# Optimization experiments

Hardware: AMD Instinct MI355X
Metric: run time of the kernel (lower is better)

Reference implementation:

```python
import jax, jax.numpy as jnp
import numpy as np


def setup_inputs() -> dict:
    key = jax.random.key(0)
    kq, kk, kv = jax.random.split(key, 3)
    B, L, H, E = 2, 2048, 16, 64
    queries = jax.random.normal(kq, (B, L, H, E), dtype=jnp.float32)
    keys = jax.random.normal(kk, (B, L, H, E), dtype=jnp.float32)
    values = jax.random.normal(kv, (B, L, H, E), dtype=jnp.float32)
    return {"queries": queries, "keys": keys, "values": values}


def reference(queries, keys, values):
    # queries: [B, L, H, E], keys: [B, S, H, E], values: [B, S, H, D]
    B, L, H, E = queries.shape
    S = keys.shape[1]
    scale = 1.0 / jnp.sqrt(jnp.asarray(E, dtype=queries.dtype))
    # scores: [B, H, L, S]
    scores = jnp.einsum('blhe,bshe->bhls', queries, keys)
    # TriangularCausalMask: mask out strictly-upper-triangular (future) positions
    causal = jnp.triu(jnp.ones((L, S), dtype=bool), k=1)
    neg_inf = jnp.asarray(-jnp.inf, dtype=scores.dtype)
    scores = jnp.where(causal[None, None, :, :], neg_inf, scores)
    A = jax.nn.softmax(scale * scores, axis=-1)  # dropout p=0.0 (eval)
    # V: [B, L, H, D]
    V = jnp.einsum('bhls,bshd->blhd', A, values)
    return V
```

## Files before the change

kernel.cpp:

```cpp
#include <hip/hip_runtime.h>


constexpr int LL = 2048, HH = 16;
constexpr float SL2E = 0.125f * 1.44269504088896340736f;
constexpr float NEG = -1e30f;
constexpr size_t PLANE = 262144;

using bf16x8 = __attribute__((ext_vector_type(8))) short;
using f32x4  = __attribute__((ext_vector_type(4))) float;

__device__ inline float fast_exp2(float x) { return __builtin_amdgcn_exp2f(x); }

__device__ inline unsigned short f2bf(float f) {
    unsigned u = __builtin_bit_cast(unsigned, f);
    return (unsigned short)((u + 0x7fffu + ((u >> 16) & 1u)) >> 16);
}
__device__ inline unsigned pk2r(float lo, float hi) {
    unsigned al = __builtin_bit_cast(unsigned, lo) + 0x8000u;
    unsigned ah = __builtin_bit_cast(unsigned, hi) + 0x8000u;
    return __builtin_amdgcn_perm(ah, al, 0x07060302u);
}
__device__ inline void gload16(const void* g, void* l) {
    __builtin_amdgcn_global_load_lds(
        (const __attribute__((address_space(1))) unsigned int*)g,
        (__attribute__((address_space(3))) unsigned int*)l, 16, 0, 0);
}

__global__ __launch_bounds__(256) void prepack(
    const float* __restrict__ K, const float* __restrict__ V,
    char* __restrict__ wsK, char* __restrict__ wsV)
{
    const int bh = blockIdx.x >> 4;
    const int chunk = blockIdx.x & 15;
    const int b = bh >> 4, h = bh & 15;
    const int s0 = chunk * 128;
    const int tid = threadIdx.x;
    const int wv = tid >> 6, lane = tid & 63;
    const int g = lane >> 4, c16 = lane & 15;

    char* outK = wsK + (size_t)bh * PLANE;
    char* outV = wsV + (size_t)bh * PLANE;

    #pragma unroll
    for (int i = 0; i < 4; ++i) {
        const int idx = i * 256 + tid;
        const int sl = idx >> 3, o = idx & 7;
        const float* src = K + (((size_t)(b * 2048 + s0 + sl)) * 16 + h) * 64 + o * 8;
        float4 f0 = *(const float4*)src;
        float4 f1 = *(const float4*)(src + 4);
        short4 lo = make_short4((short)f2bf(f0.x), (short)f2bf(f0.y),
                                (short)f2bf(f0.z), (short)f2bf(f0.w));
        short4 hi = make_short4((short)f2bf(f1.x), (short)f2bf(f1.y),
                                (short)f2bf(f1.z), (short)f2bf(f1.w));
        char* dst = outK + (s0 + sl) * 128 + ((o << 4) ^ ((sl & 7) << 4));
        *(short4*)dst = lo;
        *(short4*)(dst + 8) = hi;
    }

    const int vrow0 = wv * 4 + g;
    const float* pV = V + (((size_t)(b * 2048 + s0 + vrow0)) * 16 + h) * 64 + c16 * 4;
    const int d = c16 * 4 + g;
    #pragma unroll
    for (int it = 0; it < 8; ++it) {
        float4 vf = *(const float4*)(pV + (size_t)it * 16 * 1024);
        unsigned short a0 = f2bf(vf.x), a1 = f2bf(vf.y),
                       a2 = f2bf(vf.z), a3 = f2bf(vf.w);
        unsigned s1 = (g & 1) ? ((unsigned)a0 | ((unsigned)a2 << 16))
                              : ((unsigned)a1 | ((unsigned)a3 << 16));
        unsigned r1 = __shfl_xor(s1, 16, 64);
        if (g & 1) { a0 = (unsigned short)r1; a2 = (unsigned short)(r1 >> 16); }
        else       { a1 = (unsigned short)r1; a3 = (unsigned short)(r1 >> 16); }
        unsigned s2 = (g & 2) ? ((unsigned)a0 | ((unsigned)a1 << 16))
                              : ((unsigned)a2 | ((unsigned)a3 << 16));
        unsigned r2 = __shfl_xor(s2, 32, 64);
        if (g & 2) { a0 = (unsigned short)r2; a1 = (unsigned short)(r2 >> 16); }
        else       { a2 = (unsigned short)r2; a3 = (unsigned short)(r2 >> 16); }
        const int p_g  = 4 * (it >> 1) + wv;
        const int half = it & 1;
        char* dst = outV + (size_t)d * 4096 + chunk * 256
                  + (((p_g ^ (d & 7)) << 4) + (half << 3));
        *(short4*)dst = make_short4((short)a0, (short)a1, (short)a2, (short)a3);
    }
}

__global__ __launch_bounds__(256, 2) void attn_main(
    const float* __restrict__ Q, const char* __restrict__ wsK,
    const char* __restrict__ wsV, float* __restrict__ Out)
{
    __shared__ __align__(16) short Kb[2][8192];
    __shared__ __align__(16) short Vt[2][8192];

    const int tid  = threadIdx.x;
    const int wv   = tid >> 6;
    const int lane = tid & 63;
    const int g    = lane >> 4;
    const int c16  = lane & 15;

    const int i  = blockIdx.x;
    const int bh = ((i & 7) << 2) | ((i >> 3) & 3);
    const int qslot = i >> 5;
    const int qi = (qslot < 8) ? (15 - qslot) : (qslot - 8);
    const int b = bh >> 4, h = bh & 15;
    const int q0  = qi * 128;
    const int wq0 = q0 + wv * 32;

    bf16x8 bQ[2][2];
    #pragma unroll
    for (int qg = 0; qg < 2; ++qg) {
        const int qrow = wq0 + qg * 16 + c16;
        const float* qp = Q + ((size_t)(b * LL + qrow) * HH + h) * 64 + g * 8;
        #pragma unroll
        for (int es = 0; es < 2; ++es) {
            float4 f0 = *(const float4*)(qp + es * 32);
            float4 f1 = *(const float4*)(qp + es * 32 + 4);
            bf16x8 a;
            a[0] = f2bf(f0.x * SL2E); a[1] = f2bf(f0.y * SL2E);
            a[2] = f2bf(f0.z * SL2E); a[3] = f2bf(f0.w * SL2E);
            a[4] = f2bf(f1.x * SL2E); a[5] = f2bf(f1.y * SL2E);
            a[6] = f2bf(f1.z * SL2E); a[7] = f2bf(f1.w * SL2E);
            bQ[qg][es] = a;
        }
    }

    const short ONE = (short)0x3F80;
    const bf16x8 bOnes = {ONE, ONE, ONE, ONE, ONE, ONE, ONE, ONE};

    const char* planeK = wsK + (size_t)bh * PLANE;
    const char* planeV = wsV + (size_t)bh * PLANE;

    f32x4 Oacc[2][4];
    #pragma unroll
    for (int qg = 0; qg < 2; ++qg)
        #pragma unroll
        for (int dt = 0; dt < 4; ++dt) Oacc[qg][dt] = (f32x4){0.f, 0.f, 0.f, 0.f};
    f32x4 Lacc[2] = {(f32x4){0.f, 0.f, 0.f, 0.f}, (f32x4){0.f, 0.f, 0.f, 0.f}};

    const int ntiles = qi + 1;

    auto stage = [&](int bi, int t) {
        const char* srcK = planeK + (size_t)t * 16384 + wv * 4096 + lane * 16;
        char* dstK = (char*)&Kb[bi][0] + wv * 4096;
        #pragma unroll
        for (int k = 0; k < 4; ++k)
            gload16(srcK + k * 1024, dstK + k * 1024);
        #pragma unroll
        for (int k = 0; k < 4; ++k) {
            const int ii = wv * 4 + k;
            const char* srcV = planeV + (size_t)(4 * ii + (lane >> 4)) * 4096
                             + (size_t)t * 256 + (lane & 15) * 16;
            gload16(srcV, (char*)&Vt[bi][0] + ii * 1024);
        }
    };

    int buf = 0;
    stage(0, 0);
    for (int t = 0; t < ntiles; ++t) {
        __syncthreads();
        if (t + 1 < ntiles) stage(buf ^ 1, t + 1);

        f32x4 Sv[2][8];
        __builtin_amdgcn_s_setprio(1);
        #pragma unroll
        for (int kt = 0; kt < 8; ++kt) {
            f32x4 a0 = (f32x4){0.f, 0.f, 0.f, 0.f};
            f32x4 a1 = (f32x4){0.f, 0.f, 0.f, 0.f};
            const int krow = kt * 16 + c16;
            #pragma unroll
            for (int es = 0; es < 2; ++es) {
                const int off = krow * 128 + (((es * 64) + g * 16) ^ ((krow & 7) << 4));
                bf16x8 aK = *(const bf16x8*)((char*)&Kb[buf][0] + off);
                a0 = __builtin_amdgcn_mfma_f32_16x16x32_bf16(aK, bQ[0][es], a0, 0, 0, 0);
                a1 = __builtin_amdgcn_mfma_f32_16x16x32_bf16(aK, bQ[1][es], a1, 0, 0, 0);
            }
            Sv[0][kt] = a0; Sv[1][kt] = a1;
        }
        __builtin_amdgcn_s_setprio(0);

        const bool dia = (t == qi);
        unsigned pb[2][16];
        #pragma unroll
        for (int qg = 0; qg < 2; ++qg) {
            const int thr = 32 * wv + 16 * qg + c16;
            #pragma unroll
            for (int kt = 0; kt < 8; ++kt) {
                float x0 = Sv[qg][kt][0], x1 = Sv[qg][kt][1];
                float x2 = Sv[qg][kt][2], x3 = Sv[qg][kt][3];
                if (dia) {
                    const int k0 = 16 * kt + 4 * g;
                    x0 = (k0 + 0 <= thr) ? x0 : NEG;
                    x1 = (k0 + 1 <= thr) ? x1 : NEG;
                    x2 = (k0 + 2 <= thr) ? x2 : NEG;
                    x3 = (k0 + 3 <= thr) ? x3 : NEG;
                }
                const float p0 = fast_exp2(x0), p1 = fast_exp2(x1);
                const float p2 = fast_exp2(x2), p3 = fast_exp2(x3);
                pb[qg][2 * kt]     = pk2r(p0, p1);
                pb[qg][2 * kt + 1] = pk2r(p2, p3);
            }
        }

        __builtin_amdgcn_s_setprio(1);
        #pragma unroll
        for (int ks = 0; ks < 4; ++ks) {
            uint4 u0, u1;
            u0.x = pb[0][4 * ks]; u0.y = pb[0][4 * ks + 1];
            u0.z = pb[0][4 * ks + 2]; u0.w = pb[0][4 * ks + 3];
            u1.x = pb[1][4 * ks]; u1.y = pb[1][4 * ks + 1];
            u1.z = pb[1][4 * ks + 2]; u1.w = pb[1][4 * ks + 3];
            const bf16x8 pa0 = __builtin_bit_cast(bf16x8, u0);
            const bf16x8 pa1 = __builtin_bit_cast(bf16x8, u1);
            Lacc[0] = __builtin_amdgcn_mfma_f32_16x16x32_bf16(pa0, bOnes, Lacc[0], 0, 0, 0);
            Lacc[1] = __builtin_amdgcn_mfma_f32_16x16x32_bf16(pa1, bOnes, Lacc[1], 0, 0, 0);
            #pragma unroll
            for (int dt = 0; dt < 4; ++dt) {
                const int d = dt * 16 + c16;
                const int voff = d * 256 + ((64 * ks + 16 * g) ^ ((d & 7) << 4));
                bf16x8 bV = *(const bf16x8*)((char*)&Vt[buf][0] + voff);
                Oacc[0][dt] = __builtin_amdgcn_mfma_f32_16x16x32_bf16(pa0, bV, Oacc[0][dt], 0, 0, 0);
                Oacc[1][dt] = __builtin_amdgcn_mfma_f32_16x16x32_bf16(pa1, bV, Oacc[1][dt], 0, 0, 0);
            }
        }
        __builtin_amdgcn_s_setprio(0);
        buf ^= 1;
    }

    #pragma unroll
    for (int qg = 0; qg < 2; ++qg) {
        #pragma unroll
        for (int r = 0; r < 4; ++r) {
            const float inv = 1.0f / Lacc[qg][r];
            const int orow = wq0 + qg * 16 + g * 4 + r;
            float* op = Out + ((size_t)(b * LL + orow) * HH + h) * 64 + c16;
            #pragma unroll
            for (int dt = 0; dt < 4; ++dt)
                op[dt * 16] = Oacc[qg][dt][r] * inv;
        }
    }
}

extern "C" void kernel_launch(void* const* d_in, const int* in_sizes, int n_in,
                              void* d_out, int out_size, void* d_ws, size_t ws_size,
                              hipStream_t stream) {
    const float* Q = (const float*)d_in[0];
    const float* K = (const float*)d_in[1];
    const float* V = (const float*)d_in[2];
    float* out = (float*)d_out;
    (void)in_sizes; (void)n_in; (void)out_size; (void)ws_size;

    char* wsK = (char*)d_ws;
    char* wsV = (char*)d_ws + 32 * PLANE;
    prepack<<<512, 256, 0, stream>>>(K, V, wsK, wsV);
    attn_main<<<512, 256, 0, stream>>>(Q, wsK, wsV, out);
}
```

Before: 48.15 us.

## Split key tile across wave pairs and reduce partial outputs through LDS

Reorganizes the four waves into two query groups of 64 rows by two key halves of 64 keys. Each wave loads its K and V fragments once per tile into registers and reuses them across four query subgroups, with a cross-wave reduction of O and row sums through shared memory at the end. This aims to cut redundant LDS reads of K/V per wave, at the cost of more accumulator registers (4x4 Oacc), which may hurt occupancy, plus an extra reduction phase.

```diff
diff --git a/kernel.cpp b/kernel.cpp
--- a/kernel.cpp
+++ b/kernel.cpp
@@ -95,6 +95,8 @@
     const int lane = tid & 63;
     const int g    = lane >> 4;
     const int c16  = lane & 15;
+    const int wq   = wv >> 1;
+    const int wk   = wv & 1;
 
     const int i  = blockIdx.x;
     const int bh = ((i & 7) << 2) | ((i >> 3) & 3);
@@ -102,12 +104,12 @@
     const int qi = (qslot < 8) ? (15 - qslot) : (qslot - 8);
     const int b = bh >> 4, h = bh & 15;
     const int q0  = qi * 128;
-    const int wq0 = q0 + wv * 32;
-
-    bf16x8 bQ[2][2];
-    #pragma unroll
-    for (int qg = 0; qg < 2; ++qg) {
-        const int qrow = wq0 + qg * 16 + c16;
+    const int wqb = q0 + wq * 64;
+
+    bf16x8 bQ[4][2];
+    #pragma unroll
+    for (int qg = 0; qg < 4; ++qg) {
+        const int qrow = wqb + qg * 16 + c16;
         const float* qp = Q + ((size_t)(b * LL + qrow) * HH + h) * 64 + g * 8;
         #pragma unroll
         for (int es = 0; es < 2; ++es) {
@@ -128,12 +130,14 @@
     const char* planeK = wsK + (size_t)bh * PLANE;
     const char* planeV = wsV + (size_t)bh * PLANE;
 
-    f32x4 Oacc[2][4];
-    #pragma unroll
-    for (int qg = 0; qg < 2; ++qg)
+    f32x4 Oacc[4][4];
+    #pragma unroll
+    for (int qg = 0; qg < 4; ++qg)
         #pragma unroll
         for (int dt = 0; dt < 4; ++dt) Oacc[qg][dt] = (f32x4){0.f, 0.f, 0.f, 0.f};
-    f32x4 Lacc[2] = {(f32x4){0.f, 0.f, 0.f, 0.f}, (f32x4){0.f, 0.f, 0.f, 0.f}};
+    f32x4 Lacc[4];
+    #pragma unroll
+    for (int qg = 0; qg < 4; ++qg) Lacc[qg] = (f32x4){0.f, 0.f, 0.f, 0.f};
 
     const int ntiles = qi + 1;
 
@@ -158,35 +162,50 @@
         __syncthreads();
         if (t + 1 < ntiles) stage(buf ^ 1, t + 1);
 
-        f32x4 Sv[2][8];
-        __builtin_amdgcn_s_setprio(1);
-        #pragma unroll
-        for (int kt = 0; kt < 8; ++kt) {
-            f32x4 a0 = (f32x4){0.f, 0.f, 0.f, 0.f};
-            f32x4 a1 = (f32x4){0.f, 0.f, 0.f, 0.f};
-            const int krow = kt * 16 + c16;
+        bf16x8 aK[4][2];
+        #pragma unroll
+        for (int kt2 = 0; kt2 < 4; ++kt2) {
+            const int krow = (4 * wk + kt2) * 16 + c16;
             #pragma unroll
             for (int es = 0; es < 2; ++es) {
                 const int off = krow * 128 + (((es * 64) + g * 16) ^ ((krow & 7) << 4));
-                bf16x8 aK = *(const bf16x8*)((char*)&Kb[buf][0] + off);
-                a0 = __builtin_amdgcn_mfma_f32_16x16x32_bf16(aK, bQ[0][es], a0, 0, 0, 0);
-                a1 = __builtin_amdgcn_mfma_f32_16x16x32_bf16(aK, bQ[1][es], a1, 0, 0, 0);
-            }
-            Sv[0][kt] = a0; Sv[1][kt] = a1;
-        }
-        __builtin_amdgcn_s_setprio(0);
+                aK[kt2][es] = *(const bf16x8*)((char*)&Kb[buf][0] + off);
+            }
+        }
+        bf16x8 bV[2][4];
+        #pragma unroll
+        for (int ksl = 0; ksl < 2; ++ksl) {
+            const int ks = 2 * wk + ksl;
+            #pragma unroll
+            for (int dt = 0; dt < 4; ++dt) {
+                const int d = dt * 16 + c16;
+                const int voff = d * 256 + ((64 * ks + 16 * g) ^ ((d & 7) << 4));
+                bV[ksl][dt] = *(const bf16x8*)((char*)&Vt[buf][0] + voff);
+            }
+        }
 
         const bool dia = (t == qi);
-        unsigned pb[2][16];
-        #pragma unroll
-        for (int qg = 0; qg < 2; ++qg) {
-            const int thr = 32 * wv + 16 * qg + c16;
-            #pragma unroll
-            for (int kt = 0; kt < 8; ++kt) {
-                float x0 = Sv[qg][kt][0], x1 = Sv[qg][kt][1];
-                float x2 = Sv[qg][kt][2], x3 = Sv[qg][kt][3];
+        #pragma unroll
+        for (int qg = 0; qg < 4; ++qg) {
+            f32x4 Sv[4];
+            __builtin_amdgcn_s_setprio(1);
+            #pragma unroll
+            for (int kt2 = 0; kt2 < 4; ++kt2) {
+                f32x4 acc = (f32x4){0.f, 0.f, 0.f, 0.f};
+                acc = __builtin_amdgcn_mfma_f32_16x16x32_bf16(aK[kt2][0], bQ[qg][0], acc, 0, 0, 0);
+                acc = __builtin_amdgcn_mfma_f32_16x16x32_bf16(aK[kt2][1], bQ[qg][1], acc, 0, 0, 0);
+                Sv[kt2] = acc;
+            }
+            __builtin_amdgcn_s_setprio(0);
+
+            const int thr = wq * 64 + qg * 16 + c16;
+            unsigned pb[8];
+            #pragma unroll
+            for (int kt2 = 0; kt2 < 4; ++kt2) {
+                float x0 = Sv[kt2][0], x1 = Sv[kt2][1];
+                float x2 = Sv[kt2][2], x3 = Sv[kt2][3];
                 if (dia) {
-                    const int k0 = 16 * kt + 4 * g;
+                    const int k0 = (4 * wk + kt2) * 16 + 4 * g;
                     x0 = (k0 + 0 <= thr) ? x0 : NEG;
                     x1 = (k0 + 1 <= thr) ? x1 : NEG;
                     x2 = (k0 + 2 <= thr) ? x2 : NEG;
@@ -194,46 +213,62 @@
                 }
                 const float p0 = fast_exp2(x0), p1 = fast_exp2(x1);
                 const float p2 = fast_exp2(x2), p3 = fast_exp2(x3);
-                pb[qg][2 * kt]     = pk2r(p0, p1);
-                pb[qg][2 * kt + 1] = pk2r(p2, p3);
-            }
-        }
-
-        __builtin_amdgcn_s_setprio(1);
-        #pragma unroll
-        for (int ks = 0; ks < 4; ++ks) {
-            uint4 u0, u1;
-            u0.x = pb[0][4 * ks]; u0.y = pb[0][4 * ks + 1];
-            u0.z = pb[0][4 * ks + 2]; u0.w = pb[0][4 * ks + 3];
-            u1.x = pb[1][4 * ks]; u1.y = pb[1][4 * ks + 1];
-            u1.z = pb[1][4 * ks + 2]; u1.w = pb[1][4 * ks + 3];
-            const bf16x8 pa0 = __builtin_bit_cast(bf16x8, u0);
-            const bf16x8 pa1 = __builtin_bit_cast(bf16x8, u1);
-            Lacc[0] = __builtin_amdgcn_mfma_f32_16x16x32_bf16(pa0, bOnes, Lacc[0], 0, 0, 0);
-            Lacc[1] = __builtin_amdgcn_mfma_f32_16x16x32_bf16(pa1, bOnes, Lacc[1], 0, 0, 0);
+                pb[2 * kt2]     = pk2r(p0, p1);
+                pb[2 * kt2 + 1] = pk2r(p2, p3);
+            }
+
+            __builtin_amdgcn_s_setprio(1);
+            #pragma unroll
+            for (int ksl = 0; ksl < 2; ++ksl) {
+                uint4 u;
+                u.x = pb[4 * ksl]; u.y = pb[4 * ksl + 1];
+                u.z = pb[4 * ksl + 2]; u.w = pb[4 * ksl + 3];
+                const bf16x8 pa = __builtin_bit_cast(bf16x8, u);
+                Lacc[qg] = __builtin_amdgcn_mfma_f32_16x16x32_bf16(pa, bOnes, Lacc[qg], 0, 0, 0);
+                #pragma unroll
+                for (int dt = 0; dt < 4; ++dt)
+                    Oacc[qg][dt] = __builtin_amdgcn_mfma_f32_16x16x32_bf16(pa, bV[ksl][dt], Oacc[qg][dt], 0, 0, 0);
+            }
+            __builtin_amdgcn_s_setprio(0);
+        }
+        buf ^= 1;
+    }
+
+    __syncthreads();
+    float* Ko = (float*)&Kb[0][0];
+    float* Lo = (float*)&Vt[0][0];
+    if (wk) {
+        #pragma unroll
+        for (int qg = 0; qg < 4; ++qg) {
             #pragma unroll
             for (int dt = 0; dt < 4; ++dt) {
-                const int d = dt * 16 + c16;
-                const int voff = d * 256 + ((64 * ks + 16 * g) ^ ((d & 7) << 4));
-                bf16x8 bV = *(const bf16x8*)((char*)&Vt[buf][0] + voff);
-                Oacc[0][dt] = __builtin_amdgcn_mfma_f32_16x16x32_bf16(pa0, bV, Oacc[0][dt], 0, 0, 0);
-                Oacc[1][dt] = __builtin_amdgcn_mfma_f32_16x16x32_bf16(pa1, bV, Oacc[1][dt], 0, 0, 0);
-            }
-        }
-        __builtin_amdgcn_s_setprio(0);
-        buf ^= 1;
-    }
-
-    #pragma unroll
-    for (int qg = 0; qg < 2; ++qg) {
-        #pragma unroll
-        for (int r = 0; r < 4; ++r) {
-            const float inv = 1.0f / Lacc[qg][r];
-            const int orow = wq0 + qg * 16 + g * 4 + r;
-            float* op = Out + ((size_t)(b * LL + orow) * HH + h) * 64 + c16;
-            #pragma unroll
-            for (int dt = 0; dt < 4; ++dt)
-                op[dt * 16] = Oacc[qg][dt][r] * inv;
+                const int idx = wq * 4096 + ((((qg * 4 + g) * 4 + dt) * 16 + c16) << 2);
+                *(f32x4*)&Ko[idx] = Oacc[qg][dt];
+            }
+            if (c16 == 0)
+                *(f32x4*)&Lo[wq * 64 + qg * 16 + g * 4] = Lacc[qg];
+        }
+    }
+    __syncthreads();
+    if (!wk) {
+        #pragma unroll
+        for (int qg = 0; qg < 4; ++qg) {
+            const f32x4 lp = *(const f32x4*)&Lo[wq * 64 + qg * 16 + g * 4];
+            Lacc[qg] += lp;
+            #pragma unroll
+            for (int dt = 0; dt < 4; ++dt) {
+                const int idx = wq * 4096 + ((((qg * 4 + g) * 4 + dt) * 16 + c16) << 2);
+                Oacc[qg][dt] += *(const f32x4*)&Ko[idx];
+            }
+            #pragma unroll
+            for (int r = 0; r < 4; ++r) {
+                const float inv = 1.0f / Lacc[qg][r];
+                const int orow = q0 + wq * 64 + qg * 16 + g * 4 + r;
+                float* op = Out + ((size_t)(b * LL + orow) * HH + h) * 64 + c16;
+                #pragma unroll
+                for (int dt = 0; dt < 4; ++dt)
+                    op[dt * 16] = Oacc[qg][dt][r] * inv;
+            }
         }
     }
 }
```

Result: slower. 50.06 us (+4.0%).
